# Optimization experiments

Measured on AMD Instinct MI355X. Metric: run time of the kernel, lower is better.

## Reference

```python
import jax, jax.numpy as jnp
import numpy as np

KS = 3               # kernel_size
PAD = (KS - 1) // 2  # same padding
K2 = KS * KS
B, H, W = 4, 1024, 1024
SCALE = 1.0          # residual scale


def setup_inputs() -> dict:
    key = jax.random.key(0)
    k1, k2, k3 = jax.random.split(key, 3)
    init_dem = jax.random.normal(k1, (B, 1, H, W), jnp.float32)
    weight = jax.random.normal(k2, (B, K2, H, W), jnp.float32)          # modulation mask
    offset = jax.random.normal(k3, (B, 2 * K2, H, W), jnp.float32) * 2.0  # (dy,dx) per tap
    w = jnp.ones((1, 1, KS, KS), jnp.float32)   # nn.Parameter ones
    b = jnp.zeros((1,), jnp.float32)            # nn.Parameter zeros
    return {"init_dem": init_dem, "weight": weight, "offset": offset, "w": w, "b": b}


def _bilinear(img, y, x):
    # img: [H, W]; y, x: [H, W] fractional sample positions. Zero padding outside.
    Hh, Ww = img.shape
    y0 = jnp.floor(y)
    x0 = jnp.floor(x)

    def gather(yi, xi):
        valid = (yi >= 0) & (yi <= Hh - 1) & (xi >= 0) & (xi <= Ww - 1)
        yc = jnp.clip(yi, 0, Hh - 1).astype(jnp.int32)
        xc = jnp.clip(xi, 0, Ww - 1).astype(jnp.int32)
        return jnp.where(valid, img[yc, xc], 0.0)

    wy1 = y - y0
    wx1 = x - x0
    wy0 = 1.0 - wy1
    wx0 = 1.0 - wx1
    return (wy0 * wx0 * gather(y0, x0)
            + wy0 * wx1 * gather(y0, x0 + 1.0)
            + wy1 * wx0 * gather(y0 + 1.0, x0)
            + wy1 * wx1 * gather(y0 + 1.0, x0 + 1.0))


def reference(init_dem, weight, offset, w, b):
    # residual=True branch: zero-mean normalize the modulation mask over taps
    mask = weight - jnp.mean(weight, axis=1, keepdims=True)            # [B, K2, H, W]
    off = offset.reshape(B, K2, 2, H, W)                               # (dy, dx) per tap

    ky, kx = jnp.meshgrid(jnp.arange(KS), jnp.arange(KS), indexing="ij")
    ky = ky.reshape(-1).astype(jnp.float32)                            # [K2]
    kx = kx.reshape(-1).astype(jnp.float32)
    hh = jnp.arange(H, dtype=jnp.float32)[:, None]                     # [H, 1]
    ww = jnp.arange(W, dtype=jnp.float32)[None, :]                     # [1, W]

    # sample position for tap k at output pixel (h, w): p = p0 + k - pad + offset
    ys = (hh - PAD + ky[:, None, None])[None] + off[:, :, 0]           # [B, K2, H, W]
    xs = (ww - PAD + kx[:, None, None])[None] + off[:, :, 1]

    # vmap over batch (image varies) and taps (image shared)
    sample = jax.vmap(jax.vmap(_bilinear, in_axes=(None, 0, 0)),
                      in_axes=(0, 0, 0))(init_dem[:, 0], ys, xs)       # [B, K2, H, W]

    refined = jnp.einsum("bkhw,k->bhw", sample * mask, w.reshape(-1)) + b[0]
    return refined[:, None] + SCALE * init_dem                          # residual add
```

## Files before the change

### kernel.cpp

```cpp
#include <hip/hip_runtime.h>

#define BB 4
#define HH 1024
#define WW 1024
#define K2 9
#define PAD 1

#define R   12
#define TW  64
#define TH  8
#define RW  (TW + 2*R)
#define RH  (TH + 2*R)
#define RSZ (RW * RH)

__global__ __launch_bounds__(256) void dcn_kernel(
    const float* __restrict__ init_dem,
    const float* __restrict__ weight,
    const float* __restrict__ offset,
    const float* __restrict__ wk,
    const float* __restrict__ bias,
    float* __restrict__ out)
{
    __shared__ float region[RSZ];

    const int HW = HH * WW;

    int i    = blockIdx.x;
    int b    = (i & 7) >> 1;
    int widx = ((i >> 3) << 1) | (i & 1);
    int tile_w = widx & 15;
    int tile_h = widx >> 4;
    int w0 = tile_w * TW;
    int h0 = tile_h * TH;

    const float* img = init_dem + (size_t)b * HW;

    int tid = threadIdx.x;
#pragma unroll
    for (int it = 0; it < RSZ / 256; ++it) {
        int e = tid + it * 256;
        int r = e / RW;
        int c = e - r * RW;
        int gy = h0 - R + r;
        int gx = w0 - R + c;
        float v = 0.f;
        if ((unsigned)gy < (unsigned)HH && (unsigned)gx < (unsigned)WW)
            v = img[gy * WW + gx];
        region[e] = v;
    }
    __syncthreads();

    const int tx = tid & 63;
    const int ty = tid >> 6;
    const float bval = bias[0];

    float wgt[K2];
#pragma unroll
    for (int k = 0; k < K2; ++k) wgt[k] = wk[k];

#pragma unroll
    for (int p = 0; p < 2; ++p) {
        int h = h0 + ty + p * 4;
        int w = w0 + tx;
        int rem = h * WW + w;

        const float* wq = weight + (size_t)b * K2 * HW + rem;
        const float* oq = offset + (size_t)b * 2 * K2 * HW + rem;

        float wt[K2], dy[K2], dx[K2];
        float wsum = 0.f;
#pragma unroll
        for (int k = 0; k < K2; ++k) {
            wt[k] = __builtin_nontemporal_load(wq + (size_t)k * HW);
            dy[k] = __builtin_nontemporal_load(oq + (size_t)(2 * k) * HW);
            dx[k] = __builtin_nontemporal_load(oq + (size_t)(2 * k + 1) * HW);
            wsum += wt[k];
        }
        const float mean = wsum * (1.0f / K2);

        float acc = 0.f;
#pragma unroll
        for (int k = 0; k < K2; ++k) {
            float ys = (float)(h - PAD + k / 3) + dy[k];
            float xs = (float)(w - PAD + k % 3) + dx[k];

            float y0f = floorf(ys);
            float x0f = floorf(xs);
            float wy1 = ys - y0f;
            float wx1 = xs - x0f;
            float wy0 = 1.f - wy1;
            float wx0 = 1.f - wx1;

            int y0g = (int)y0f;
            int x0g = (int)x0f;
            int y0l = y0g - (h0 - R);
            int x0l = x0g - (w0 - R);

            float v00, v01, v10, v11;
            bool fast = (y0l >= 0) & (y0l < RH - 1) & (x0l >= 0) & (x0l < RW - 1);
            if (fast) {
                int base = y0l * RW + x0l;
                v00 = region[base];
                v01 = region[base + 1];
                v10 = region[base + RW];
                v11 = region[base + RW + 1];
            } else {
                int y1g = y0g + 1;
                int x1g = x0g + 1;
                bool y0v = (y0g >= 0) & (y0g < HH);
                bool y1v = (y1g >= 0) & (y1g < HH);
                bool x0v = (x0g >= 0) & (x0g < WW);
                bool x1v = (x1g >= 0) & (x1g < WW);
                int yc0 = min(max(y0g, 0), HH - 1);
                int yc1 = min(max(y1g, 0), HH - 1);
                int xc0 = min(max(x0g, 0), WW - 1);
                int xc1 = min(max(x1g, 0), WW - 1);
                v00 = (y0v & x0v) ? img[(size_t)yc0 * WW + xc0] : 0.f;
                v01 = (y0v & x1v) ? img[(size_t)yc0 * WW + xc1] : 0.f;
                v10 = (y1v & x0v) ? img[(size_t)yc1 * WW + xc0] : 0.f;
                v11 = (y1v & x1v) ? img[(size_t)yc1 * WW + xc1] : 0.f;
            }

            float samp = wy0 * (wx0 * v00 + wx1 * v01)
                       + wy1 * (wx0 * v10 + wx1 * v11);
            acc += samp * (wt[k] - mean) * wgt[k];
        }

        float resid = region[(ty + p * 4 + R) * RW + (tx + R)];
        float rres = acc + bval + resid;
        __builtin_nontemporal_store(rres, out + (size_t)b * HW + rem);
    }
}

extern "C" void kernel_launch(void* const* d_in, const int* in_sizes, int n_in,
                              void* d_out, int out_size, void* d_ws, size_t ws_size,
                              hipStream_t stream) {
    const float* init_dem = (const float*)d_in[0];
    const float* weight   = (const float*)d_in[1];
    const float* offset   = (const float*)d_in[2];
    const float* wk       = (const float*)d_in[3];
    const float* bias     = (const float*)d_in[4];
    float* out            = (float*)d_out;

    const int nblocks = BB * (WW / TW) * (HH / TH);
    dcn_kernel<<<dim3(nblocks), dim3(256), 0, stream>>>(init_dem, weight, offset, wk, bias, out);
}
```

Baseline: 102.6 us.

## Vectorize per-thread work to four pixels with float4 loads and wider tiles

Each thread now handles four adjacent pixels in a row, using 128-bit nontemporal loads for the weight and offset planes and a 128-bit store for the output. The tile widens to 128x8, so the shared halo region is proportionally smaller relative to the tile. The mean subtraction is rewritten algebraically as accA - mean*accB, which lets taps be processed as they stream in instead of buffering all 27 values first. This adds register pressure and changes the rounding order slightly.

```diff
diff --git a/kernel.cpp b/kernel.cpp
--- a/kernel.cpp
+++ b/kernel.cpp
@@ -6,12 +6,14 @@
 #define K2 9
 #define PAD 1
 
-#define R   12
-#define TW  64
-#define TH  8
-#define RW  (TW + 2*R)
-#define RH  (TH + 2*R)
+#define TW 128
+#define TH 8
+#define R  12
+#define RW (TW + 2*R)
+#define RH (TH + 2*R)
 #define RSZ (RW * RH)
+
+typedef float f32x4 __attribute__((ext_vector_type(4)));
 
 __global__ __launch_bounds__(256) void dcn_kernel(
     const float* __restrict__ init_dem,
@@ -28,8 +30,8 @@
     int i    = blockIdx.x;
     int b    = (i & 7) >> 1;
     int widx = ((i >> 3) << 1) | (i & 1);
-    int tile_w = widx & 15;
-    int tile_h = widx >> 4;
+    int tile_w = widx & 7;
+    int tile_h = widx >> 3;
     int w0 = tile_w * TW;
     int h0 = tile_h * TH;
 
@@ -50,39 +52,34 @@
     }
     __syncthreads();
 
-    const int tx = tid & 63;
-    const int ty = tid >> 6;
-    const float bval = bias[0];
+    const int tx4 = (tid & 31) << 2;
+    const int ty  = tid >> 5;
+    const int h   = h0 + ty;
+    const int w   = w0 + tx4;
+    const int rem = h * WW + w;
 
-    float wgt[K2];
-#pragma unroll
-    for (int k = 0; k < K2; ++k) wgt[k] = wk[k];
+    const float* wq = weight + (size_t)b * K2 * HW + rem;
+    const float* oq = offset + (size_t)b * 2 * K2 * HW + rem;
+
+    float accA[4] = {0.f, 0.f, 0.f, 0.f};
+    float accB[4] = {0.f, 0.f, 0.f, 0.f};
+    float msum[4] = {0.f, 0.f, 0.f, 0.f};
 
 #pragma unroll
-    for (int p = 0; p < 2; ++p) {
-        int h = h0 + ty + p * 4;
-        int w = w0 + tx;
-        int rem = h * WW + w;
+    for (int k = 0; k < K2; ++k) {
+        f32x4 wtv = __builtin_nontemporal_load((const f32x4*)(wq + (size_t)k * HW));
+        f32x4 dyv = __builtin_nontemporal_load((const f32x4*)(oq + (size_t)(2 * k) * HW));
+        f32x4 dxv = __builtin_nontemporal_load((const f32x4*)(oq + (size_t)(2 * k + 1) * HW));
+        const float wkk = wk[k];
+        const int ky = k / 3, kx = k % 3;
 
-        const float* wq = weight + (size_t)b * K2 * HW + rem;
-        const float* oq = offset + (size_t)b * 2 * K2 * HW + rem;
+#pragma unroll
+        for (int p = 0; p < 4; ++p) {
+            float dy = dyv[p], dx = dxv[p], wt = wtv[p];
+            msum[p] += wt;
 
-        float wt[K2], dy[K2], dx[K2];
-        float wsum = 0.f;
-#pragma unroll
-        for (int k = 0; k < K2; ++k) {
-            wt[k] = __builtin_nontemporal_load(wq + (size_t)k * HW);
-            dy[k] = __builtin_nontemporal_load(oq + (size_t)(2 * k) * HW);
-            dx[k] = __builtin_nontemporal_load(oq + (size_t)(2 * k + 1) * HW);
-            wsum += wt[k];
-        }
-        const float mean = wsum * (1.0f / K2);
-
-        float acc = 0.f;
-#pragma unroll
-        for (int k = 0; k < K2; ++k) {
-            float ys = (float)(h - PAD + k / 3) + dy[k];
-            float xs = (float)(w - PAD + k % 3) + dx[k];
+            float ys = (float)(h - PAD + ky) + dy;
+            float xs = (float)(w + p - PAD + kx) + dx;
 
             float y0f = floorf(ys);
             float x0f = floorf(xs);
@@ -123,13 +120,21 @@
 
             float samp = wy0 * (wx0 * v00 + wx1 * v01)
                        + wy1 * (wx0 * v10 + wx1 * v11);
-            acc += samp * (wt[k] - mean) * wgt[k];
+            float sw = samp * wkk;
+            accA[p] += sw * wt;
+            accB[p] += sw;
         }
+    }
 
-        float resid = region[(ty + p * 4 + R) * RW + (tx + R)];
-        float rres = acc + bval + resid;
-        __builtin_nontemporal_store(rres, out + (size_t)b * HW + rem);
+    const float bval = bias[0];
+    f32x4 res;
+#pragma unroll
+    for (int p = 0; p < 4; ++p) {
+        float mean  = msum[p] * (1.0f / K2);
+        float resid = region[(ty + R) * RW + (tx4 + R + p)];
+        res[p] = accA[p] - mean * accB[p] + bval + resid;
     }
+    __builtin_nontemporal_store(res, (f32x4*)(out + (size_t)b * HW + rem));
 }
 
 extern "C" void kernel_launch(void* const* d_in, const int* in_sizes, int n_in,
```

After: 191.1 us. 1.86x slower.

## Stream taps in groups of three and fold mean subtraction algebraically

Applied to the files above, without the earlier changes.

Replaces the two-pass computation (load all 27 mask and offset values, take the mean, then sample) with a single streaming pass over three groups of three taps. The mask mean is split out algebraically as accA - mean*accB, so no tap needs the mean before the sum is complete. This is meant to lower register pressure and let loads overlap with sampling. In exchange it may reduce memory-level parallelism, since fewer loads are in flight at once, and it changes floating-point rounding slightly. The tap weights are now read from wk inside the loop instead of being hoisted.

```diff
diff --git a/kernel.cpp b/kernel.cpp
--- a/kernel.cpp
+++ b/kernel.cpp
@@ -54,10 +54,6 @@
     const int ty = tid >> 6;
     const float bval = bias[0];
 
-    float wgt[K2];
-#pragma unroll
-    for (int k = 0; k < K2; ++k) wgt[k] = wk[k];
-
 #pragma unroll
     for (int p = 0; p < 2; ++p) {
         int h = h0 + ty + p * 4;
@@ -67,67 +63,78 @@
         const float* wq = weight + (size_t)b * K2 * HW + rem;
         const float* oq = offset + (size_t)b * 2 * K2 * HW + rem;
 
-        float wt[K2], dy[K2], dx[K2];
-        float wsum = 0.f;
+        float accA = 0.f;
+        float accB = 0.f;
+        float msum = 0.f;
+
 #pragma unroll
-        for (int k = 0; k < K2; ++k) {
-            wt[k] = __builtin_nontemporal_load(wq + (size_t)k * HW);
-            dy[k] = __builtin_nontemporal_load(oq + (size_t)(2 * k) * HW);
-            dx[k] = __builtin_nontemporal_load(oq + (size_t)(2 * k + 1) * HW);
-            wsum += wt[k];
-        }
-        const float mean = wsum * (1.0f / K2);
-
-        float acc = 0.f;
+        for (int kg = 0; kg < 3; ++kg) {
+            float wt[3], dy[3], dx[3];
 #pragma unroll
-        for (int k = 0; k < K2; ++k) {
-            float ys = (float)(h - PAD + k / 3) + dy[k];
-            float xs = (float)(w - PAD + k % 3) + dx[k];
-
-            float y0f = floorf(ys);
-            float x0f = floorf(xs);
-            float wy1 = ys - y0f;
-            float wx1 = xs - x0f;
-            float wy0 = 1.f - wy1;
-            float wx0 = 1.f - wx1;
-
-            int y0g = (int)y0f;
-            int x0g = (int)x0f;
-            int y0l = y0g - (h0 - R);
-            int x0l = x0g - (w0 - R);
-
-            float v00, v01, v10, v11;
-            bool fast = (y0l >= 0) & (y0l < RH - 1) & (x0l >= 0) & (x0l < RW - 1);
-            if (fast) {
-                int base = y0l * RW + x0l;
-                v00 = region[base];
-                v01 = region[base + 1];
-                v10 = region[base + RW];
-                v11 = region[base + RW + 1];
-            } else {
-                int y1g = y0g + 1;
-                int x1g = x0g + 1;
-                bool y0v = (y0g >= 0) & (y0g < HH);
-                bool y1v = (y1g >= 0) & (y1g < HH);
-                bool x0v = (x0g >= 0) & (x0g < WW);
-                bool x1v = (x1g >= 0) & (x1g < WW);
-                int yc0 = min(max(y0g, 0), HH - 1);
-                int yc1 = min(max(y1g, 0), HH - 1);
-                int xc0 = min(max(x0g, 0), WW - 1);
-                int xc1 = min(max(x1g, 0), WW - 1);
-                v00 = (y0v & x0v) ? img[(size_t)yc0 * WW + xc0] : 0.f;
-                v01 = (y0v & x1v) ? img[(size_t)yc0 * WW + xc1] : 0.f;
-                v10 = (y1v & x0v) ? img[(size_t)yc1 * WW + xc0] : 0.f;
-                v11 = (y1v & x1v) ? img[(size_t)yc1 * WW + xc1] : 0.f;
+            for (int j = 0; j < 3; ++j) {
+                int k = kg * 3 + j;
+                wt[j] = __builtin_nontemporal_load(wq + (size_t)k * HW);
+                dy[j] = __builtin_nontemporal_load(oq + (size_t)(2 * k) * HW);
+                dx[j] = __builtin_nontemporal_load(oq + (size_t)(2 * k + 1) * HW);
             }
 
-            float samp = wy0 * (wx0 * v00 + wx1 * v01)
-                       + wy1 * (wx0 * v10 + wx1 * v11);
-            acc += samp * (wt[k] - mean) * wgt[k];
+#pragma unroll
+            for (int j = 0; j < 3; ++j) {
+                int k = kg * 3 + j;
+                int ky = k / 3, kx = k % 3;
+                msum += wt[j];
+
+                float ys = (float)(h - PAD + ky) + dy[j];
+                float xs = (float)(w - PAD + kx) + dx[j];
+
+                float y0f = floorf(ys);
+                float x0f = floorf(xs);
+                float wy1 = ys - y0f;
+                float wx1 = xs - x0f;
+                float wy0 = 1.f - wy1;
+                float wx0 = 1.f - wx1;
+
+                int y0g = (int)y0f;
+                int x0g = (int)x0f;
+                int y0l = y0g - (h0 - R);
+                int x0l = x0g - (w0 - R);
+
+                float v00, v01, v10, v11;
+                bool fast = (y0l >= 0) & (y0l < RH - 1) & (x0l >= 0) & (x0l < RW - 1);
+                if (fast) {
+                    int base = y0l * RW + x0l;
+                    v00 = region[base];
+                    v01 = region[base + 1];
+                    v10 = region[base + RW];
+                    v11 = region[base + RW + 1];
+                } else {
+                    int y1g = y0g + 1;
+                    int x1g = x0g + 1;
+                    bool y0v = (y0g >= 0) & (y0g < HH);
+                    bool y1v = (y1g >= 0) & (y1g < HH);
+                    bool x0v = (x0g >= 0) & (x0g < WW);
+                    bool x1v = (x1g >= 0) & (x1g < WW);
+                    int yc0 = min(max(y0g, 0), HH - 1);
+                    int yc1 = min(max(y1g, 0), HH - 1);
+                    int xc0 = min(max(x0g, 0), WW - 1);
+                    int xc1 = min(max(x1g, 0), WW - 1);
+                    v00 = (y0v & x0v) ? img[(size_t)yc0 * WW + xc0] : 0.f;
+                    v01 = (y0v & x1v) ? img[(size_t)yc0 * WW + xc1] : 0.f;
+                    v10 = (y1v & x0v) ? img[(size_t)yc1 * WW + xc0] : 0.f;
+                    v11 = (y1v & x1v) ? img[(size_t)yc1 * WW + xc1] : 0.f;
+                }
+
+                float samp = wy0 * (wx0 * v00 + wx1 * v01)
+                           + wy1 * (wx0 * v10 + wx1 * v11);
+                float sw = samp * wk[k];
+                accA += sw * wt[j];
+                accB += sw;
+            }
         }
 
+        float mean  = msum * (1.0f / K2);
         float resid = region[(ty + p * 4 + R) * RW + (tx + R)];
-        float rres = acc + bval + resid;
+        float rres  = accA - mean * accB + bval + resid;
         __builtin_nontemporal_store(rres, out + (size_t)b * HW + rem);
     }
 }
```

After: 117.0 us. +14.0%, slower.
